# Performance work log

Hardware: AMD Instinct MI355X
Metric: run time of the kernel (lower is better)

The kernel has to match this reference:

```python
import jax, jax.numpy as jnp
import numpy as np

TOPK = 10
NUM_CLASSES = 80
ALPHA = 1.0
BETA = 6.0
EPS = 1e-8


def setup_inputs() -> dict:
    key = jax.random.key(0)
    ks = jax.random.split(key, 6)
    B, A, NB, C = 32, 8400, 32, 80
    pred_scores = jax.random.uniform(ks[0], (B, A, C), dtype=jnp.float32)
    # anchor grid for 640x640 image, strides 8/16/32 -> 6400+1600+400 = 8400 points
    pts = []
    for s in (8, 16, 32):
        n = 640 // s
        xs = (jnp.arange(n, dtype=jnp.float32) + 0.5) * s
        gy, gx = jnp.meshgrid(xs, xs, indexing='ij')
        pts.append(jnp.stack([gx.ravel(), gy.ravel()], axis=-1))
    anchor_points = jnp.concatenate(pts, axis=0)  # (8400, 2)
    # predicted boxes: anchor point +- random extents (xyxy)
    off = jax.random.uniform(ks[1], (B, A, 4), minval=4.0, maxval=64.0, dtype=jnp.float32)
    pred_boxes = jnp.concatenate([anchor_points[None] - off[..., :2],
                                  anchor_points[None] + off[..., 2:]], axis=-1)
    gt_cxcy = jax.random.uniform(ks[2], (B, NB, 2), minval=64.0, maxval=576.0, dtype=jnp.float32)
    gt_wh = jax.random.uniform(ks[3], (B, NB, 2), minval=16.0, maxval=256.0, dtype=jnp.float32)
    gt_boxes = jnp.concatenate([gt_cxcy - gt_wh / 2, gt_cxcy + gt_wh / 2], axis=-1)
    gt_labels = jax.random.randint(ks[4], (B, NB, 1), 0, C)
    gt_mask = jax.random.uniform(ks[5], (B, NB, 1)) < 0.8  # padded-GT validity mask
    return {"pred_scores": pred_scores, "pred_boxes": pred_boxes,
            "anchor_points": anchor_points, "gt_labels": gt_labels,
            "gt_boxes": gt_boxes, "gt_mask": gt_mask}


def reference(pred_scores, pred_boxes, anchor_points, gt_labels, gt_boxes, gt_mask):
    B, A, C = pred_scores.shape
    NB = gt_boxes.shape[1]
    dt = pred_scores.dtype
    gt_valid = gt_mask[..., 0]  # (B, NB) bool

    # --- step 3 mask: anchor centers inside GT boxes ---
    lt = gt_boxes[:, :, None, :2]  # (B, NB, 1, 2)
    rb = gt_boxes[:, :, None, 2:]
    ap = anchor_points[None, None]  # (1, 1, A, 2)
    d = jnp.minimum((ap - lt).min(-1), (rb - ap).min(-1))  # (B, NB, A)
    mask_in = d > 1e-8
    valid = mask_in & gt_valid[:, :, None]
    vf = valid.astype(dt)

    # --- classification score of each anchor for each GT's class ---
    cls = gt_labels[..., 0].astype(jnp.int32)  # (B, NB)
    bcs = jnp.take_along_axis(pred_scores, cls[:, None, :], axis=2)  # (B, A, NB)
    bcs = jnp.swapaxes(bcs, 1, 2) * vf  # (B, NB, A)

    # --- pairwise IoU (xyxy) between GT and predicted boxes ---
    b1 = gt_boxes[:, :, None, :]   # (B, NB, 1, 4)
    b2 = pred_boxes[:, None, :, :]  # (B, 1, A, 4)
    iw = jnp.clip(jnp.minimum(b1[..., 2], b2[..., 2]) - jnp.maximum(b1[..., 0], b2[..., 0]), 0)
    ih = jnp.clip(jnp.minimum(b1[..., 3], b2[..., 3]) - jnp.maximum(b1[..., 1], b2[..., 1]), 0)
    inter = iw * ih
    a1 = (b1[..., 2] - b1[..., 0]) * (b1[..., 3] - b1[..., 1])
    a2 = (b2[..., 2] - b2[..., 0]) * (b2[..., 3] - b2[..., 1])
    ious = jnp.maximum(inter / (a1 + a2 - inter + 1e-10), 0.0) * vf  # (B, NB, A)

    align = jnp.power(bcs, ALPHA) * jnp.power(ious, BETA)  # (B, NB, A)

    # --- step 2: top-k candidates per GT (scatter-add counts, drop dupes) ---
    _, topk_idx = jax.lax.top_k(align, TOPK)  # (B, NB, K)
    topk_idx = jnp.where(gt_valid[:, :, None], topk_idx, 0)
    bi = jnp.arange(B)[:, None, None]
    gi = jnp.arange(NB)[None, :, None]
    counts = jnp.zeros((B, NB, A), jnp.int32).at[bi, gi, topk_idx].add(1)
    topk_mask = jnp.where(counts > 1, 0, counts).astype(dt)
    mask = topk_mask * vf  # (B, NB, A)

    # --- step 4: anchors matched to multiple GTs keep the highest-IoU GT ---
    fg = mask.sum(axis=1)  # (B, A)
    best_gt = jnp.argmax(ious, axis=1)  # (B, A)
    onehot_best = (best_gt[:, None, :] == jnp.arange(NB)[None, :, None]).astype(dt)
    mask = jnp.where(fg[:, None, :] > 1, onehot_best, mask)
    fg = mask.sum(axis=1)
    tgt_idx = jnp.argmax(mask, axis=1)  # (B, A)

    # --- gather targets ---
    target_labels = jnp.clip(jnp.take_along_axis(cls, tgt_idx, axis=1), 0, NUM_CLASSES)  # (B, A)
    target_boxes = jnp.take_along_axis(gt_boxes, tgt_idx[..., None], axis=1)  # (B, A, 4)
    target_scores = jax.nn.one_hot(target_labels, NUM_CLASSES, dtype=dt)
    target_scores = target_scores * (fg[..., None] > 0)

    # --- normalize scores by aligned metric ---
    align = align * mask
    pos_align = align.max(axis=-1, keepdims=True)           # (B, NB, 1)
    pos_iou = (ious * mask).max(axis=-1, keepdims=True)     # (B, NB, 1)
    norm = (align * pos_iou / (pos_align + EPS)).max(axis=-2)[..., None]  # (B, A, 1)
    target_scores = target_scores * norm

    return target_labels, target_boxes, target_scores, fg > 0
```

## Files before the change

kernel.cpp:

```cpp
#include <hip/hip_runtime.h>
#include <cstdint>
#include <cstddef>

#define BB 32
#define AA 8400
#define NBB 32
#define CC 80
#define TOPKN 10

__global__ __launch_bounds__(256) void gt_topk_kernel(
    const float* __restrict__ pred_scores, const float* __restrict__ pred_boxes,
    const int* __restrict__ gt_labels, const float* __restrict__ gt_boxes,
    const int* __restrict__ gt_mask,
    int* __restrict__ tk, int* __restrict__ posA, int* __restrict__ posI,
    float* __restrict__ out) {
  const int j = blockIdx.x, b = blockIdx.y, t = threadIdx.x;
  const int g = b * NBB + j;
  if (t == 0) { posA[g] = 0; posI[g] = 0; }

  {
    const int NA = BB * AA;
    const int labels4 = NA / 4;
    const int boxes4_end = labels4 + NA;
    const int total4 = labels4 + NA + NA * 20 + NA / 4;
    float4* o4 = reinterpret_cast<float4*>(out);
    for (int idx = (g << 8) + t; idx < total4; idx += 1024 * 256) {
      if (idx < labels4) {
        const int fb = (idx * 4) / AA;
        int lab = gt_labels[fb * NBB];
        lab = min(max(lab, 0), 80);
        const float lf = (float)lab;
        o4[idx] = make_float4(lf, lf, lf, lf);
      } else if (idx < boxes4_end) {
        const int aidx = idx - labels4;
        const int fb = aidx / AA;
        o4[idx] =
            *reinterpret_cast<const float4*>(gt_boxes + (size_t)fb * NBB * 4);
      } else {
        o4[idx] = make_float4(0.f, 0.f, 0.f, 0.f);
      }
    }
  }

  const float gx0 = gt_boxes[g * 4 + 0], gy0 = gt_boxes[g * 4 + 1];
  const float gx1 = gt_boxes[g * 4 + 2], gy1 = gt_boxes[g * 4 + 3];
  const int cls = gt_labels[g];
  const bool valid = (gt_mask[g] != 0);
  const float ga1 = (gx1 - gx0) * (gy1 - gy0);

  unsigned long long tkkey[TOPKN];
#pragma unroll
  for (int k = 0; k < TOPKN; k++) tkkey[k] = 0ull;

  if (valid) {
    const int strides[3] = {8, 16, 32};
    const int grids[3] = {80, 40, 20};
    const int offs[3] = {0, 6400, 8000};
    for (int lvl = 0; lvl < 3; lvl++) {
      const float s = (float)strides[lvl];
      const int n = grids[lvl], off = offs[lvl];
      int lx = max(0, (int)floorf(gx0 / s - 0.5f) - 1);
      int hx = min(n - 1, (int)ceilf(gx1 / s - 0.5f) + 1);
      int ly = max(0, (int)floorf(gy0 / s - 0.5f) - 1);
      int hy = min(n - 1, (int)ceilf(gy1 / s - 0.5f) + 1);
      if (hx < lx || hy < ly) continue;
      const int w = hx - lx + 1;
      const int m = w * (hy - ly + 1);
      for (int i = t; i < m; i += 256) {
        const int ix = lx + i % w;
        const int iy = ly + i / w;
        const float apx = ((float)ix + 0.5f) * s;
        const float apy = ((float)iy + 0.5f) * s;
        const float d = fminf(fminf(apx - gx0, apy - gy0),
                              fminf(gx1 - apx, gy1 - apy));
        if (!(d > 1e-8f)) continue;
        const int a = off + iy * n + ix;
        const float* pb = pred_boxes + ((size_t)b * AA + a) * 4;
        const float p0 = pb[0], p1 = pb[1], p2 = pb[2], p3 = pb[3];
        const float iw = fmaxf(fminf(gx1, p2) - fmaxf(gx0, p0), 0.0f);
        const float ih = fmaxf(fminf(gy1, p3) - fmaxf(gy0, p1), 0.0f);
        const float inter = iw * ih;
        const float a2 = (p2 - p0) * (p3 - p1);
        const float iou = fmaxf(inter / (ga1 + a2 - inter + 1e-10f), 0.0f);
        const float sc = pred_scores[((size_t)b * AA + a) * CC + cls];
        const float i2 = iou * iou;
        const float align_v = sc * i2 * i2 * i2;
        const unsigned long long key =
            ((unsigned long long)__float_as_uint(align_v) << 32) |
            (unsigned int)(AA - a);
        if (key > tkkey[TOPKN - 1]) {
          tkkey[TOPKN - 1] = key;
#pragma unroll
          for (int k = TOPKN - 1; k > 0; k--) {
            if (tkkey[k] > tkkey[k - 1]) {
              unsigned long long tmp = tkkey[k];
              tkkey[k] = tkkey[k - 1];
              tkkey[k - 1] = tmp;
            }
          }
        }
      }
    }
  }

  __shared__ unsigned long long s_key[256][TOPKN + 1];
#pragma unroll
  for (int k = 0; k < TOPKN; k++) s_key[t][k] = tkkey[k];
  __syncthreads();

  for (int stride = 128; stride >= 1; stride >>= 1) {
    if (t < stride) {
      unsigned long long mk[TOPKN];
      int p = 0, q = 0;
#pragma unroll
      for (int k = 0; k < TOPKN; k++) {
        const unsigned long long k1 = s_key[t][p], k2 = s_key[t + stride][q];
        if (k1 >= k2) { mk[k] = k1; p++; } else { mk[k] = k2; q++; }
      }
#pragma unroll
      for (int k = 0; k < TOPKN; k++) s_key[t][k] = mk[k];
    }
    __syncthreads();
  }

  if (t < TOPKN) {
    const unsigned long long key = s_key[0][t];
    tk[g * TOPKN + t] = (key != 0ull) ? (AA - (int)(key & 0xffffffffu)) : -1;
  }
}

__global__ __launch_bounds__(64) void assign_sparse_kernel(
    const float* __restrict__ pred_scores, const float* __restrict__ pred_boxes,
    const float* __restrict__ anchor_points, const int* __restrict__ gt_labels,
    const float* __restrict__ gt_boxes, const int* __restrict__ gt_mask,
    const int* __restrict__ tk,
    int* __restrict__ resj, float* __restrict__ resAl,
    int* __restrict__ posA, int* __restrict__ posI) {
  const int j = blockIdx.x, b = blockIdx.y, t = threadIdx.x;

  __shared__ float sbox[NBB][4];
  __shared__ int scls[NBB];
  __shared__ int svalid[NBB];
  __shared__ int sa[NBB * TOPKN];

  if (t < NBB) {
    const int g = b * NBB + t;
    sbox[t][0] = gt_boxes[g * 4 + 0];
    sbox[t][1] = gt_boxes[g * 4 + 1];
    sbox[t][2] = gt_boxes[g * 4 + 2];
    sbox[t][3] = gt_boxes[g * 4 + 3];
    scls[t] = gt_labels[g];
    svalid[t] = (gt_mask[g] != 0) ? 1 : 0;
  }
  for (int e = t; e < NBB * TOPKN; e += 64) sa[e] = tk[b * NBB * TOPKN + e];
  __syncthreads();

  if (t >= TOPKN) return;
  const int a = sa[j * TOPKN + t];
  if (a < 0) return;

  int cnt = 0;
  for (int q = 0; q < NBB * TOPKN; q++) cnt += (sa[q] == a) ? 1 : 0;

  const float apx = anchor_points[a * 2 + 0];
  const float apy = anchor_points[a * 2 + 1];
  const float* pb = pred_boxes + ((size_t)b * AA + a) * 4;
  const float p0 = pb[0], p1 = pb[1], p2 = pb[2], p3 = pb[3];
  const float a2 = (p2 - p0) * (p3 - p1);

  int jj;
  float iou_f;
  if (cnt == 1) {
    jj = j;
    const float gx0 = sbox[j][0], gy0 = sbox[j][1];
    const float gx1 = sbox[j][2], gy1 = sbox[j][3];
    const float iw = fmaxf(fminf(gx1, p2) - fmaxf(gx0, p0), 0.0f);
    const float ih = fmaxf(fminf(gy1, p3) - fmaxf(gy0, p1), 0.0f);
    const float inter = iw * ih;
    const float a1 = (gx1 - gx0) * (gy1 - gy0);
    iou_f = fmaxf(inter / (a1 + a2 - inter + 1e-10f), 0.0f);
  } else {
    float best_iou = -1.0f;
    int best_j = 0;
    for (int jq = 0; jq < NBB; jq++) {
      const float gx0 = sbox[jq][0], gy0 = sbox[jq][1];
      const float gx1 = sbox[jq][2], gy1 = sbox[jq][3];
      const float d = fminf(fminf(apx - gx0, apy - gy0),
                            fminf(gx1 - apx, gy1 - apy));
      float iou = 0.0f;
      if (svalid[jq] && d > 1e-8f) {
        const float iw = fmaxf(fminf(gx1, p2) - fmaxf(gx0, p0), 0.0f);
        const float ih = fmaxf(fminf(gy1, p3) - fmaxf(gy0, p1), 0.0f);
        const float inter = iw * ih;
        const float a1 = (gx1 - gx0) * (gy1 - gy0);
        iou = fmaxf(inter / (a1 + a2 - inter + 1e-10f), 0.0f);
      }
      if (iou > best_iou) { best_iou = iou; best_j = jq; }
    }
    jj = best_j;
    iou_f = best_iou;
  }

  const float sc = pred_scores[((size_t)b * AA + a) * CC + scls[jj]];
  const float i2 = iou_f * iou_f;
  const float align_v = sc * i2 * i2 * i2;
  const int e = (b * NBB + j) * TOPKN + t;
  resj[e] = jj;
  resAl[e] = align_v;
  atomicMax(&posA[b * NBB + jj], __float_as_int(align_v));
  atomicMax(&posI[b * NBB + jj], __float_as_int(iou_f));
}

__global__ __launch_bounds__(256) void scatter_out_kernel(
    const int* __restrict__ gt_labels, const float* __restrict__ gt_boxes,
    const int* __restrict__ tk, const int* __restrict__ resj,
    const float* __restrict__ resAl, const int* __restrict__ posA,
    const int* __restrict__ posI, float* __restrict__ out) {
  const int e = blockIdx.x * 256 + threadIdx.x;
  if (e >= BB * NBB * TOPKN) return;
  const int a = tk[e];
  if (a < 0) return;
  const int b = e / (NBB * TOPKN);
  const int jj = resj[e];
  const float align_v = resAl[e];
  const float pa = __int_as_float(posA[b * NBB + jj]);
  const float pi = __int_as_float(posI[b * NBB + jj]);
  const float norm = align_v * pi / (pa + 1e-8f);
  int label = gt_labels[b * NBB + jj];
  label = min(max(label, 0), 80);
  const size_t aidx = (size_t)b * AA + a;

  out[aidx] = (float)label;
  *reinterpret_cast<float4*>(out + (size_t)BB * AA + aidx * 4) =
      *reinterpret_cast<const float4*>(gt_boxes + ((size_t)b * NBB + jj) * 4);
  if (label < CC)
    out[(size_t)BB * AA * 5 + aidx * CC + label] = norm;
  out[(size_t)BB * AA * 85 + aidx] = 1.0f;
}

extern "C" void kernel_launch(void* const* d_in, const int* in_sizes, int n_in,
                              void* d_out, int out_size, void* d_ws, size_t ws_size,
                              hipStream_t stream) {
  const float* pred_scores = (const float*)d_in[0];
  const float* pred_boxes = (const float*)d_in[1];
  const float* anchor_points = (const float*)d_in[2];
  const int* gt_labels = (const int*)d_in[3];
  const float* gt_boxes = (const float*)d_in[4];
  const int* gt_mask = (const int*)d_in[5];
  float* out = (float*)d_out;
  char* ws = (char*)d_ws;

  const size_t off_tk = 0;
  const size_t off_posA = off_tk + (size_t)BB * NBB * TOPKN * 4;
  const size_t off_posI = off_posA + 4096;
  const size_t off_resj = off_posI + 4096;
  const size_t off_resAl = off_resj + (size_t)BB * NBB * TOPKN * 4;

  int* tk = (int*)(ws + off_tk);
  int* posA = (int*)(ws + off_posA);
  int* posI = (int*)(ws + off_posI);
  int* resj = (int*)(ws + off_resj);
  float* resAl = (float*)(ws + off_resAl);

  dim3 g1(NBB, BB);
  gt_topk_kernel<<<g1, 256, 0, stream>>>(pred_scores, pred_boxes, gt_labels,
                                         gt_boxes, gt_mask, tk, posA, posI,
                                         out);

  dim3 g2(NBB, BB);
  assign_sparse_kernel<<<g2, 64, 0, stream>>>(
      pred_scores, pred_boxes, anchor_points, gt_labels, gt_boxes, gt_mask,
      tk, resj, resAl, posA, posI);

  const int ncand = BB * NBB * TOPKN;
  scatter_out_kernel<<<(ncand + 255) / 256, 256, 0, stream>>>(
      gt_labels, gt_boxes, tk, resj, resAl, posA, posI, out);
}
```

Baseline: 48.91 us.

## Fuse assign and scatter kernels with per-batch redundant resolution and nontemporal stores

Merges the assignment and scatter kernels into one. Each block now redundantly resolves all 320 candidates of its batch and computes the per-GT max align and IoU in shared memory, which removes the global atomics, the workspace round trip and one kernel launch. The bulk output initialization also switches to nontemporal stores to cut cache pollution. The cost is 32x redundant candidate resolution per batch, including extra scattered loads of pred_boxes and pred_scores.

```diff
diff --git a/kernel.cpp b/kernel.cpp
--- a/kernel.cpp
+++ b/kernel.cpp
@@ -7,38 +7,40 @@
 #define NBB 32
 #define CC 80
 #define TOPKN 10
+#define NCAND (NBB * TOPKN)
+
+typedef float nfloat4 __attribute__((ext_vector_type(4)));
 
 __global__ __launch_bounds__(256) void gt_topk_kernel(
     const float* __restrict__ pred_scores, const float* __restrict__ pred_boxes,
     const int* __restrict__ gt_labels, const float* __restrict__ gt_boxes,
     const int* __restrict__ gt_mask,
-    int* __restrict__ tk, int* __restrict__ posA, int* __restrict__ posI,
-    float* __restrict__ out) {
+    int* __restrict__ tk, float* __restrict__ out) {
   const int j = blockIdx.x, b = blockIdx.y, t = threadIdx.x;
   const int g = b * NBB + j;
-  if (t == 0) { posA[g] = 0; posI[g] = 0; }
 
   {
     const int NA = BB * AA;
     const int labels4 = NA / 4;
     const int boxes4_end = labels4 + NA;
     const int total4 = labels4 + NA + NA * 20 + NA / 4;
-    float4* o4 = reinterpret_cast<float4*>(out);
+    nfloat4* o4 = reinterpret_cast<nfloat4*>(out);
     for (int idx = (g << 8) + t; idx < total4; idx += 1024 * 256) {
+      nfloat4 v;
       if (idx < labels4) {
         const int fb = (idx * 4) / AA;
         int lab = gt_labels[fb * NBB];
         lab = min(max(lab, 0), 80);
         const float lf = (float)lab;
-        o4[idx] = make_float4(lf, lf, lf, lf);
+        v = (nfloat4){lf, lf, lf, lf};
       } else if (idx < boxes4_end) {
         const int aidx = idx - labels4;
         const int fb = aidx / AA;
-        o4[idx] =
-            *reinterpret_cast<const float4*>(gt_boxes + (size_t)fb * NBB * 4);
+        v = *reinterpret_cast<const nfloat4*>(gt_boxes + (size_t)fb * NBB * 4);
       } else {
-        o4[idx] = make_float4(0.f, 0.f, 0.f, 0.f);
-      }
+        v = (nfloat4){0.f, 0.f, 0.f, 0.f};
+      }
+      __builtin_nontemporal_store(v, &o4[idx]);
     }
   }
 
@@ -129,19 +131,22 @@
   }
 }
 
-__global__ __launch_bounds__(64) void assign_sparse_kernel(
+__global__ __launch_bounds__(64) void resolve_scatter_kernel(
     const float* __restrict__ pred_scores, const float* __restrict__ pred_boxes,
     const float* __restrict__ anchor_points, const int* __restrict__ gt_labels,
     const float* __restrict__ gt_boxes, const int* __restrict__ gt_mask,
-    const int* __restrict__ tk,
-    int* __restrict__ resj, float* __restrict__ resAl,
-    int* __restrict__ posA, int* __restrict__ posI) {
+    const int* __restrict__ tk, float* __restrict__ out) {
   const int j = blockIdx.x, b = blockIdx.y, t = threadIdx.x;
 
   __shared__ float sbox[NBB][4];
   __shared__ int scls[NBB];
   __shared__ int svalid[NBB];
-  __shared__ int sa[NBB * TOPKN];
+  __shared__ int sa[NCAND];
+  __shared__ int ejj[NCAND];
+  __shared__ float eal[NCAND];
+  __shared__ float eiu[NCAND];
+  __shared__ float sposA[NBB];
+  __shared__ float sposI[NBB];
 
   if (t < NBB) {
     const int g = b * NBB + t;
@@ -152,90 +157,95 @@
     scls[t] = gt_labels[g];
     svalid[t] = (gt_mask[g] != 0) ? 1 : 0;
   }
-  for (int e = t; e < NBB * TOPKN; e += 64) sa[e] = tk[b * NBB * TOPKN + e];
-  __syncthreads();
-
-  if (t >= TOPKN) return;
-  const int a = sa[j * TOPKN + t];
-  if (a < 0) return;
-
-  int cnt = 0;
-  for (int q = 0; q < NBB * TOPKN; q++) cnt += (sa[q] == a) ? 1 : 0;
-
-  const float apx = anchor_points[a * 2 + 0];
-  const float apy = anchor_points[a * 2 + 1];
-  const float* pb = pred_boxes + ((size_t)b * AA + a) * 4;
-  const float p0 = pb[0], p1 = pb[1], p2 = pb[2], p3 = pb[3];
-  const float a2 = (p2 - p0) * (p3 - p1);
-
-  int jj;
-  float iou_f;
-  if (cnt == 1) {
-    jj = j;
-    const float gx0 = sbox[j][0], gy0 = sbox[j][1];
-    const float gx1 = sbox[j][2], gy1 = sbox[j][3];
-    const float iw = fmaxf(fminf(gx1, p2) - fmaxf(gx0, p0), 0.0f);
-    const float ih = fmaxf(fminf(gy1, p3) - fmaxf(gy0, p1), 0.0f);
-    const float inter = iw * ih;
-    const float a1 = (gx1 - gx0) * (gy1 - gy0);
-    iou_f = fmaxf(inter / (a1 + a2 - inter + 1e-10f), 0.0f);
-  } else {
-    float best_iou = -1.0f;
-    int best_j = 0;
-    for (int jq = 0; jq < NBB; jq++) {
-      const float gx0 = sbox[jq][0], gy0 = sbox[jq][1];
-      const float gx1 = sbox[jq][2], gy1 = sbox[jq][3];
-      const float d = fminf(fminf(apx - gx0, apy - gy0),
-                            fminf(gx1 - apx, gy1 - apy));
-      float iou = 0.0f;
-      if (svalid[jq] && d > 1e-8f) {
-        const float iw = fmaxf(fminf(gx1, p2) - fmaxf(gx0, p0), 0.0f);
-        const float ih = fmaxf(fminf(gy1, p3) - fmaxf(gy0, p1), 0.0f);
-        const float inter = iw * ih;
-        const float a1 = (gx1 - gx0) * (gy1 - gy0);
-        iou = fmaxf(inter / (a1 + a2 - inter + 1e-10f), 0.0f);
-      }
-      if (iou > best_iou) { best_iou = iou; best_j = jq; }
-    }
-    jj = best_j;
-    iou_f = best_iou;
-  }
-
-  const float sc = pred_scores[((size_t)b * AA + a) * CC + scls[jj]];
-  const float i2 = iou_f * iou_f;
-  const float align_v = sc * i2 * i2 * i2;
-  const int e = (b * NBB + j) * TOPKN + t;
-  resj[e] = jj;
-  resAl[e] = align_v;
-  atomicMax(&posA[b * NBB + jj], __float_as_int(align_v));
-  atomicMax(&posI[b * NBB + jj], __float_as_int(iou_f));
-}
-
-__global__ __launch_bounds__(256) void scatter_out_kernel(
-    const int* __restrict__ gt_labels, const float* __restrict__ gt_boxes,
-    const int* __restrict__ tk, const int* __restrict__ resj,
-    const float* __restrict__ resAl, const int* __restrict__ posA,
-    const int* __restrict__ posI, float* __restrict__ out) {
-  const int e = blockIdx.x * 256 + threadIdx.x;
-  if (e >= BB * NBB * TOPKN) return;
-  const int a = tk[e];
-  if (a < 0) return;
-  const int b = e / (NBB * TOPKN);
-  const int jj = resj[e];
-  const float align_v = resAl[e];
-  const float pa = __int_as_float(posA[b * NBB + jj]);
-  const float pi = __int_as_float(posI[b * NBB + jj]);
-  const float norm = align_v * pi / (pa + 1e-8f);
-  int label = gt_labels[b * NBB + jj];
-  label = min(max(label, 0), 80);
-  const size_t aidx = (size_t)b * AA + a;
-
-  out[aidx] = (float)label;
-  *reinterpret_cast<float4*>(out + (size_t)BB * AA + aidx * 4) =
-      *reinterpret_cast<const float4*>(gt_boxes + ((size_t)b * NBB + jj) * 4);
-  if (label < CC)
-    out[(size_t)BB * AA * 5 + aidx * CC + label] = norm;
-  out[(size_t)BB * AA * 85 + aidx] = 1.0f;
+  for (int e = t; e < NCAND; e += 64) sa[e] = tk[b * NCAND + e];
+  __syncthreads();
+
+  for (int e = t; e < NCAND; e += 64) {
+    const int a = sa[e];
+    if (a < 0) { ejj[e] = -1; continue; }
+    const int q = e / TOPKN;
+
+    int cnt = 0;
+    for (int i = 0; i < NCAND; i++) cnt += (sa[i] == a) ? 1 : 0;
+
+    const float apx = anchor_points[a * 2 + 0];
+    const float apy = anchor_points[a * 2 + 1];
+    const float* pb = pred_boxes + ((size_t)b * AA + a) * 4;
+    const float p0 = pb[0], p1 = pb[1], p2 = pb[2], p3 = pb[3];
+    const float a2 = (p2 - p0) * (p3 - p1);
+
+    int jj;
+    float iou_f;
+    if (cnt == 1) {
+      jj = q;
+      const float gx0 = sbox[q][0], gy0 = sbox[q][1];
+      const float gx1 = sbox[q][2], gy1 = sbox[q][3];
+      const float iw = fmaxf(fminf(gx1, p2) - fmaxf(gx0, p0), 0.0f);
+      const float ih = fmaxf(fminf(gy1, p3) - fmaxf(gy0, p1), 0.0f);
+      const float inter = iw * ih;
+      const float a1 = (gx1 - gx0) * (gy1 - gy0);
+      iou_f = fmaxf(inter / (a1 + a2 - inter + 1e-10f), 0.0f);
+    } else {
+      float best_iou = -1.0f;
+      int best_j = 0;
+      for (int jq = 0; jq < NBB; jq++) {
+        const float gx0 = sbox[jq][0], gy0 = sbox[jq][1];
+        const float gx1 = sbox[jq][2], gy1 = sbox[jq][3];
+        const float d = fminf(fminf(apx - gx0, apy - gy0),
+                              fminf(gx1 - apx, gy1 - apy));
+        float iou = 0.0f;
+        if (svalid[jq] && d > 1e-8f) {
+          const float iw = fmaxf(fminf(gx1, p2) - fmaxf(gx0, p0), 0.0f);
+          const float ih = fmaxf(fminf(gy1, p3) - fmaxf(gy0, p1), 0.0f);
+          const float inter = iw * ih;
+          const float a1 = (gx1 - gx0) * (gy1 - gy0);
+          iou = fmaxf(inter / (a1 + a2 - inter + 1e-10f), 0.0f);
+        }
+        if (iou > best_iou) { best_iou = iou; best_j = jq; }
+      }
+      jj = best_j;
+      iou_f = best_iou;
+    }
+
+    const float sc = pred_scores[((size_t)b * AA + a) * CC + scls[jj]];
+    const float i2 = iou_f * iou_f;
+    ejj[e] = jj;
+    eal[e] = sc * i2 * i2 * i2;
+    eiu[e] = iou_f;
+  }
+  __syncthreads();
+
+  if (t < NBB) {
+    float mA = 0.0f, mI = 0.0f;
+    for (int i = 0; i < NCAND; i++) {
+      if (ejj[i] == t) {
+        mA = fmaxf(mA, eal[i]);
+        mI = fmaxf(mI, eiu[i]);
+      }
+    }
+    sposA[t] = mA;
+    sposI[t] = mI;
+  }
+  __syncthreads();
+
+  if (t < TOPKN) {
+    const int e = j * TOPKN + t;
+    const int a = sa[e];
+    if (a >= 0) {
+      const int jj = ejj[e];
+      const float norm = eal[e] * sposI[jj] / (sposA[jj] + 1e-8f);
+      int label = scls[jj];
+      label = min(max(label, 0), 80);
+      const size_t aidx = (size_t)b * AA + a;
+
+      out[aidx] = (float)label;
+      *reinterpret_cast<float4*>(out + (size_t)BB * AA + aidx * 4) =
+          *reinterpret_cast<const float4*>(&sbox[jj][0]);
+      if (label < CC)
+        out[(size_t)BB * AA * 5 + aidx * CC + label] = norm;
+      out[(size_t)BB * AA * 85 + aidx] = 1.0f;
+    }
+  }
 }
 
 extern "C" void kernel_launch(void* const* d_in, const int* in_sizes, int n_in,
@@ -250,29 +260,14 @@
   float* out = (float*)d_out;
   char* ws = (char*)d_ws;
 
-  const size_t off_tk = 0;
-  const size_t off_posA = off_tk + (size_t)BB * NBB * TOPKN * 4;
-  const size_t off_posI = off_posA + 4096;
-  const size_t off_resj = off_posI + 4096;
-  const size_t off_resAl = off_resj + (size_t)BB * NBB * TOPKN * 4;
-
-  int* tk = (int*)(ws + off_tk);
-  int* posA = (int*)(ws + off_posA);
-  int* posI = (int*)(ws + off_posI);
-  int* resj = (int*)(ws + off_resj);
-  float* resAl = (float*)(ws + off_resAl);
+  int* tk = (int*)ws;
 
   dim3 g1(NBB, BB);
   gt_topk_kernel<<<g1, 256, 0, stream>>>(pred_scores, pred_boxes, gt_labels,
-                                         gt_boxes, gt_mask, tk, posA, posI,
-                                         out);
+                                         gt_boxes, gt_mask, tk, out);
 
   dim3 g2(NBB, BB);
-  assign_sparse_kernel<<<g2, 64, 0, stream>>>(
+  resolve_scatter_kernel<<<g2, 64, 0, stream>>>(
       pred_scores, pred_boxes, anchor_points, gt_labels, gt_boxes, gt_mask,
-      tk, resj, resAl, posA, posI);
-
-  const int ncand = BB * NBB * TOPKN;
-  scatter_out_kernel<<<(ncand + 255) / 256, 256, 0, stream>>>(
-      gt_labels, gt_boxes, tk, resj, resAl, posA, posI, out);
+      tk, out);
 }
```

After: 101.7 us. 108% more time.
